# Kernel tuning notes

Measured on AMD Instinct MI355X. Metric: run time of the kernel, lower is better.

The kernel has to match this reference:

```python
import jax, jax.numpy as jnp
import numpy as np

GROUP_SIZES = [16, 16, 16, 16]
K = 2
TEMPERATURE = 1.0
NEG = float(np.finfo(np.float32).min)  # torch.finfo(dtype).min


def setup_inputs() -> dict:
    key = jax.random.key(0)
    k1, k2, k3 = jax.random.split(key, 3)
    B, S, D, E, G = 8, 4096, 1024, 64, len(GROUP_SIZES)
    x = jax.random.normal(k1, (B, S, D), dtype=jnp.float32)
    W_group = jax.random.normal(k2, (G, D), dtype=jnp.float32) * 0.02
    W_expert = jax.random.normal(k3, (E, D), dtype=jnp.float32) * 0.02
    return {"x": x, "W_group": W_group, "W_expert": W_expert}


def reference(x, W_group, W_expert):
    E = W_expert.shape[0]
    # group id of each expert (contiguous ranges) -- static
    expert_group = jnp.asarray(np.repeat(np.arange(len(GROUP_SIZES)), GROUP_SIZES))  # [E]

    # gate logits (no bias), temperature scaling
    expert_logits = jnp.einsum('bsd,ed->bse', x, W_expert) * (1.0 / TEMPERATURE)  # [B,S,E]
    group_logits = jnp.einsum('bsd,gd->bsg', x, W_group)                          # [B,S,G]
    group_probs = jax.nn.softmax(group_logits, axis=-1)
    g_idx = jnp.argmax(group_probs, axis=-1)                                      # [B,S]

    # mask experts outside the selected group's contiguous range
    mask = expert_group[None, None, :] != g_idx[..., None]                        # [B,S,E] bool
    mdt = mask.astype(expert_logits.dtype)
    masked_logits = mdt * NEG + (1.0 - mdt) * expert_logits

    probs_full = jax.nn.softmax(masked_logits, axis=-1)                           # [B,S,E]
    topk_vals, idx = jax.lax.top_k(masked_logits, K)                              # [B,S,K]
    scores = jax.nn.softmax(topk_vals, axis=-1)

    # aux stats (no_grad in original)
    importance = jax.lax.stop_gradient(jnp.mean(probs_full, axis=(0, 1)))         # [E]
    counts = jnp.zeros((E,), probs_full.dtype).at[idx.reshape(-1)].add(1.0)       # [E]
    load = counts / jnp.maximum(jnp.sum(counts), 1.0)
    return (idx, scores, probs_full, importance, load)
```

## Files before the change

kernel.cpp:

```cpp
#include <hip/hip_runtime.h>
#include <math.h>

#define TOKENS   32768
#define DDIM     1024
#define TPB      64
#define NBLOCKS  (TOKENS / TPB)

#define OFF_SCORES 65536
#define OFF_PROBS  131072
#define OFF_IMP    2228224
#define OFF_LOAD   2228288

#define NSLOT 16

typedef __attribute__((ext_vector_type(8))) short  short8;
typedef __attribute__((ext_vector_type(4))) float  f32x4;
typedef __attribute__((ext_vector_type(4))) int    intx4;

__device__ __attribute__((aligned(16))) short wfrag[32 * 5 * 3 * 64 * 8];

__device__ inline unsigned rne_hi(float x) {
  unsigned u = __float_as_uint(x);
  unsigned r = u + 0x7fffu + ((u >> 16) & 1u);
  return r & 0xffff0000u;
}

__device__ inline void split3(const float* xv, short8& f1, short8& f2, short8& f3) {
  int o1[4], o2[4], o3[4];
  #pragma unroll
  for (int p = 0; p < 4; ++p) {
    float x0 = xv[2*p], x1 = xv[2*p+1];
    unsigned h0 = rne_hi(x0), h1 = rne_hi(x1);
    o1[p] = (int)((h0 >> 16) | (h1 & 0xffff0000u));
    float r0 = x0 - __uint_as_float(h0);
    float r1 = x1 - __uint_as_float(h1);
    unsigned g0 = rne_hi(r0), g1 = rne_hi(r1);
    o2[p] = (int)((g0 >> 16) | (g1 & 0xffff0000u));
    float s0 = r0 - __uint_as_float(g0);
    float s1 = r1 - __uint_as_float(g1);
    unsigned w0 = rne_hi(s0), w1 = rne_hi(s1);
    o3[p] = (int)((w0 >> 16) | (w1 & 0xffff0000u));
  }
  intx4 t1 = {o1[0], o1[1], o1[2], o1[3]};
  intx4 t2 = {o2[0], o2[1], o2[2], o2[3]};
  intx4 t3 = {o3[0], o3[1], o3[2], o3[3]};
  f1 = __builtin_bit_cast(short8, t1);
  f2 = __builtin_bit_cast(short8, t2);
  f3 = __builtin_bit_cast(short8, t3);
}

__global__ void prep_kernel(const float* __restrict__ Wg, const float* __restrict__ We,
                            float* __restrict__ ws) {
  const int nt   = blockIdx.x >> 5;
  const int ks   = blockIdx.x & 31;
  const int lane = threadIdx.x & 63;
  if (blockIdx.x < 32) ws[blockIdx.x * 64 + lane] = 0.f;
  const int row  = nt * 16 + (lane & 15);
  const int k0   = ks * 32 + (lane >> 4) * 8;
  float xv[8];
  #pragma unroll
  for (int j = 0; j < 8; ++j) {
    float v = 0.f;
    if (row < 64)      v = We[(size_t)row * DDIM + k0 + j];
    else if (row < 68) v = Wg[(size_t)(row - 64) * DDIM + k0 + j];
    xv[j] = v;
  }
  short8 f1, f2, f3;
  split3(xv, f1, f2, f3);
  short8* dst = (short8*)wfrag + (((size_t)ks * 5 + nt) * 3) * 64 + lane;
  dst[0]   = f1;
  dst[64]  = f2;
  dst[128] = f3;
}

__global__ __launch_bounds__(256)
__attribute__((amdgpu_waves_per_eu(2)))
void router_kernel(const float* __restrict__ x,
                   float* __restrict__ out,
                   float* __restrict__ ws) {
  __shared__ __attribute__((aligned(16))) char smem[61440 + 256];
  float*  el     = (float*)smem;
  short8* bstage = (short8*)smem;
  int*    cnt    = (int*)(smem + 61440);
  const int tid    = threadIdx.x;
  const int lane   = tid & 63;
  const int wv     = tid >> 6;
  const int khalf  = wv >> 1;
  const int mhalf  = wv & 1;
  const int quad   = lane >> 4;
  const int m      = lane & 15;
  const int tokblk = blockIdx.x * TPB;

  if (tid < 64) cnt[tid] = 0;

  const float* apb = x + (size_t)(tokblk + mhalf * 32 + m) * DDIM + khalf * 512 + quad * 8;
  const short8* wsrc = (const short8*)wfrag;

  f32x4 ahi[2][5], alo[2][5];
  #pragma unroll
  for (int mt = 0; mt < 2; ++mt)
    #pragma unroll
    for (int nt = 0; nt < 5; ++nt) { ahi[mt][nt] = 0.f; alo[mt][nt] = 0.f; }

  float4 cur[4], nxt[4];
  #pragma unroll
  for (int mt = 0; mt < 2; ++mt) {
    const float* p = apb + (size_t)(mt * 16) * DDIM;
    cur[mt * 2]     = *(const float4*)(p);
    cur[mt * 2 + 1] = *(const float4*)(p + 4);
  }

  {
    short8 breg[8];
    #pragma unroll
    for (int j = 0; j < 8; ++j) {
      const int c = wv + 4 * j;
      if (c < 30) {
        const int ksg = (c < 15) ? 0 : 16;
        const int fr  = (c < 15) ? c : c - 15;
        breg[j] = wsrc[((size_t)ksg * 15 + fr) * 64 + lane];
      }
    }
    #pragma unroll
    for (int j = 0; j < 8; ++j) {
      const int c = wv + 4 * j;
      if (c < 30) bstage[c * 64 + lane] = breg[j];
    }
  }
  __syncthreads();

  for (int ks = 0; ks < 16; ++ks) {
    const int pb = ks & 1;
    short8 breg[8];
    if (ks < 15) {
      #pragma unroll
      for (int j = 0; j < 8; ++j) {
        const int c = wv + 4 * j;
        if (c < 30) {
          const int ksg = (c < 15) ? (ks + 1) : (16 + ks + 1);
          const int fr  = (c < 15) ? c : c - 15;
          breg[j] = wsrc[((size_t)ksg * 15 + fr) * 64 + lane];
        }
      }
    }
    const int kpf = (ks + 1 < 16) ? (ks + 1) : 15;
    #pragma unroll
    for (int mt = 0; mt < 2; ++mt) {
      const float* p = apb + (size_t)(mt * 16) * DDIM + kpf * 32;
      nxt[mt * 2]     = *(const float4*)(p);
      nxt[mt * 2 + 1] = *(const float4*)(p + 4);
    }
    short8 fa[2][3];
    #pragma unroll
    for (int mt = 0; mt < 2; ++mt) {
      float av[8] = {cur[mt*2].x, cur[mt*2].y, cur[mt*2].z, cur[mt*2].w,
                     cur[mt*2+1].x, cur[mt*2+1].y, cur[mt*2+1].z, cur[mt*2+1].w};
      split3(av, fa[mt][0], fa[mt][1], fa[mt][2]);
    }
    const short8* bbase = &bstage[(size_t)pb * 1920 + (size_t)khalf * 15 * 64 + lane];
    short8 fb0 = bbase[0], fb1 = bbase[64], fb2 = bbase[128];
    #pragma unroll
    for (int nt = 0; nt < 5; ++nt) {
      short8 n0, n1, n2;
      if (nt < 4) {
        n0 = bbase[(nt + 1) * 192];
        n1 = bbase[(nt + 1) * 192 + 64];
        n2 = bbase[(nt + 1) * 192 + 128];
      }
      #pragma unroll
      for (int mt = 0; mt < 2; ++mt) {
        ahi[mt][nt] = __builtin_amdgcn_mfma_f32_16x16x32_bf16(fa[mt][0], fb0, ahi[mt][nt], 0, 0, 0);
        f32x4 c = alo[mt][nt];
        c = __builtin_amdgcn_mfma_f32_16x16x32_bf16(fa[mt][0], fb1, c, 0, 0, 0);
        c = __builtin_amdgcn_mfma_f32_16x16x32_bf16(fa[mt][1], fb0, c, 0, 0, 0);
        c = __builtin_amdgcn_mfma_f32_16x16x32_bf16(fa[mt][1], fb1, c, 0, 0, 0);
        c = __builtin_amdgcn_mfma_f32_16x16x32_bf16(fa[mt][0], fb2, c, 0, 0, 0);
        c = __builtin_amdgcn_mfma_f32_16x16x32_bf16(fa[mt][2], fb0, c, 0, 0, 0);
        c = __builtin_amdgcn_mfma_f32_16x16x32_bf16(fa[mt][1], fb2, c, 0, 0, 0);
        c = __builtin_amdgcn_mfma_f32_16x16x32_bf16(fa[mt][2], fb1, c, 0, 0, 0);
        alo[mt][nt] = c;
      }
      if (nt < 4) { fb0 = n0; fb1 = n1; fb2 = n2; }
    }
    if (ks < 15) {
      #pragma unroll
      for (int j = 0; j < 8; ++j) {
        const int c = wv + 4 * j;
        if (c < 30) bstage[(size_t)(pb ^ 1) * 1920 + c * 64 + lane] = breg[j];
      }
      __syncthreads();
    }
    #pragma unroll
    for (int i = 0; i < 4; ++i) cur[i] = nxt[i];
  }

  if (khalf == 1) {
    #pragma unroll
    for (int mt = 0; mt < 2; ++mt)
      #pragma unroll
      for (int nt = 0; nt < 5; ++nt)
        #pragma unroll
        for (int r = 0; r < 4; ++r)
          el[(mhalf * 32 + mt * 16 + quad * 4 + r) * 88 + nt * 16 + m] = ahi[mt][nt][r] + alo[mt][nt][r];
  }
  __syncthreads();
  if (khalf == 0) {
    #pragma unroll
    for (int mt = 0; mt < 2; ++mt)
      #pragma unroll
      for (int nt = 0; nt < 5; ++nt)
        #pragma unroll
        for (int r = 0; r < 4; ++r) {
          const int idx = (mhalf * 32 + mt * 16 + quad * 4 + r) * 88 + nt * 16 + m;
          el[idx] += ahi[mt][nt][r] + alo[mt][nt][r];
        }
  }
  __syncthreads();

  if (tid < TPB) {
    const int t = tid;
    float* row = el + t * 88;
    const float g0 = row[64], g1 = row[65], g2 = row[66], g3 = row[67];
    int g = 0; float gb = g0;
    if (g1 > gb) { g = 1; gb = g1; }
    if (g2 > gb) { g = 2; gb = g2; }
    if (g3 > gb) { g = 3; gb = g3; }
    const int base = g << 4;
    float l[16];
    #pragma unroll
    for (int e = 0; e < 16; ++e) l[e] = row[base + e];
    int i1 = 0; float v1 = l[0];
    #pragma unroll
    for (int e = 1; e < 16; ++e) if (l[e] > v1) { i1 = e; v1 = l[e]; }
    int i2 = -1; float v2 = 0.f;
    #pragma unroll
    for (int e = 0; e < 16; ++e) {
      if (e == i1) continue;
      if (i2 < 0 || l[e] > v2) { i2 = e; v2 = l[e]; }
    }
    float pr[16]; float s = 0.f;
    #pragma unroll
    for (int e = 0; e < 16; ++e) { pr[e] = expf(l[e] - v1); s += pr[e]; }
    const float inv = 1.f / s;
    #pragma unroll
    for (int c = 0; c < 64; ++c) row[c] = 0.f;
    #pragma unroll
    for (int e = 0; e < 16; ++e) row[base + e] = pr[e] * inv;
    const size_t T = (size_t)tokblk + t;
    out[2*T]     = (float)(base + i1);
    out[2*T + 1] = (float)(base + i2);
    const float e2 = expf(v2 - v1);
    const float si = 1.f / (1.f + e2);
    out[OFF_SCORES + 2*T]     = si;
    out[OFF_SCORES + 2*T + 1] = e2 * si;
    atomicAdd(&cnt[base + i1], 1);
    atomicAdd(&cnt[base + i2], 1);
  }
  __syncthreads();

  for (int i = tid; i < TPB * 64; i += 256) {
    const int t = i >> 6, c = i & 63;
    out[OFF_PROBS + (((size_t)(tokblk + t)) << 6) + c] = el[t * 88 + c];
  }
  if (tid < 64) {
    const int e = tid;
    float s = 0.f;
    #pragma unroll 4
    for (int t = 0; t < TPB; ++t) s += el[t * 88 + e];
    const int slot = (blockIdx.x & (NSLOT - 1)) * 128;
    atomicAdd(&ws[slot + e], s);
    atomicAdd(&ws[slot + 64 + e], (float)cnt[e]);
  }
}

__global__ void finalize_kernel(const float* __restrict__ ws, float* __restrict__ out) {
  const int e = threadIdx.x;
  if (e < 64) {
    float imp = 0.f, cf = 0.f;
    #pragma unroll
    for (int s = 0; s < NSLOT; ++s) {
      imp += ws[s * 128 + e];
      cf  += ws[s * 128 + 64 + e];
    }
    out[OFF_IMP  + e] = imp * (1.0f / 32768.0f);
    out[OFF_LOAD + e] = cf  * (1.0f / 65536.0f);
  }
}

extern "C" void kernel_launch(void* const* d_in, const int* in_sizes, int n_in,
                              void* d_out, int out_size, void* d_ws, size_t ws_size,
                              hipStream_t stream) {
  (void)in_sizes; (void)n_in; (void)out_size; (void)ws_size;
  const float* x  = (const float*)d_in[0];
  const float* Wg = (const float*)d_in[1];
  const float* We = (const float*)d_in[2];
  float* out = (float*)d_out;
  float* ws  = (float*)d_ws;
  hipLaunchKernelGGL(prep_kernel, dim3(160), dim3(64), 0, stream, Wg, We, ws);
  hipLaunchKernelGGL(router_kernel, dim3(NBLOCKS), dim3(256), 0, stream, x, out, ws);
  hipLaunchKernelGGL(finalize_kernel, dim3(1), dim3(64), 0, stream, ws, out);
}
```

Before: 206.5 us.

## Stage weight fragments with direct global-to-LDS loads and fuse finalize via last-block counter

Pads the weight fragment layout to 16 fragments per k-step so each wave can issue 16-byte global_load_lds copies straight into shared memory. This replaces the register round-trip of load-then-store staging. It also folds the finalize kernel into the router kernel: a last-block-done atomic counter lets the final block reduce the importance and load slots, which saves one kernel launch. The costs are a slightly larger LDS footprint, an extra zero fragment to load, and added atomic/fence synchronisation at kernel end.

```diff
diff --git a/kernel.cpp b/kernel.cpp
--- a/kernel.cpp
+++ b/kernel.cpp
@@ -17,7 +17,13 @@
 typedef __attribute__((ext_vector_type(4))) float  f32x4;
 typedef __attribute__((ext_vector_type(4))) int    intx4;
 
-__device__ __attribute__((aligned(16))) short wfrag[32 * 5 * 3 * 64 * 8];
+__device__ __attribute__((aligned(16))) short wfrag[32 * 16 * 64 * 8];
+
+__device__ inline void stage16(const void* g, void* l) {
+  __builtin_amdgcn_global_load_lds(
+      (const __attribute__((address_space(1))) void*)g,
+      (__attribute__((address_space(3))) void*)l, 16, 0, 0);
+}
 
 __device__ inline unsigned rne_hi(float x) {
   unsigned u = __float_as_uint(x);
@@ -55,6 +61,7 @@
   const int ks   = blockIdx.x & 31;
   const int lane = threadIdx.x & 63;
   if (blockIdx.x < 32) ws[blockIdx.x * 64 + lane] = 0.f;
+  if (blockIdx.x == 0 && threadIdx.x == 0) ((unsigned*)ws)[2048] = 0u;
   const int row  = nt * 16 + (lane & 15);
   const int k0   = ks * 32 + (lane >> 4) * 8;
   float xv[8];
@@ -67,10 +74,14 @@
   }
   short8 f1, f2, f3;
   split3(xv, f1, f2, f3);
-  short8* dst = (short8*)wfrag + (((size_t)ks * 5 + nt) * 3) * 64 + lane;
+  short8* dst = (short8*)wfrag + ((size_t)ks * 16 + nt * 3) * 64 + lane;
   dst[0]   = f1;
   dst[64]  = f2;
   dst[128] = f3;
+  if (nt == 4) {
+    short8 z = {};
+    ((short8*)wfrag)[((size_t)ks * 16 + 15) * 64 + lane] = z;
+  }
 }
 
 __global__ __launch_bounds__(256)
@@ -78,10 +89,10 @@
 void router_kernel(const float* __restrict__ x,
                    float* __restrict__ out,
                    float* __restrict__ ws) {
-  __shared__ __attribute__((aligned(16))) char smem[61440 + 256];
+  __shared__ __attribute__((aligned(16))) char smem[65536 + 384];
   float*  el     = (float*)smem;
   short8* bstage = (short8*)smem;
-  int*    cnt    = (int*)(smem + 61440);
+  int*    cnt    = (int*)(smem + 65536);
   const int tid    = threadIdx.x;
   const int lane   = tid & 63;
   const int wv     = tid >> 6;
@@ -94,7 +105,7 @@
   if (tid < 64) cnt[tid] = 0;
 
   const float* apb = x + (size_t)(tokblk + mhalf * 32 + m) * DDIM + khalf * 512 + quad * 8;
-  const short8* wsrc = (const short8*)wfrag;
+  const short* wsrc = wfrag;
 
   f32x4 ahi[2][5], alo[2][5];
   #pragma unroll
@@ -110,45 +121,33 @@
     cur[mt * 2 + 1] = *(const float4*)(p + 4);
   }
 
-  {
-    short8 breg[8];
-    #pragma unroll
-    for (int j = 0; j < 8; ++j) {
-      const int c = wv + 4 * j;
-      if (c < 30) {
-        const int ksg = (c < 15) ? 0 : 16;
-        const int fr  = (c < 15) ? c : c - 15;
-        breg[j] = wsrc[((size_t)ksg * 15 + fr) * 64 + lane];
-      }
-    }
-    #pragma unroll
-    for (int j = 0; j < 8; ++j) {
-      const int c = wv + 4 * j;
-      if (c < 30) bstage[c * 64 + lane] = breg[j];
-    }
+  #pragma unroll
+  for (int j = 0; j < 8; ++j) {
+    const int c = wv + 4 * j;
+    const int G = ((c < 16) ? 0 : 16) * 16 + (c & 15) * 1 + ((c < 16) ? 0 : 0) * 0;
+    const int gstep = (c < 16) ? 0 : 16;
+    const short* gs = wsrc + ((size_t)(gstep * 16 + (c & 15)) * 64 + lane) * 8;
+    stage16(gs, smem + c * 1024);
+    (void)G;
   }
   __syncthreads();
 
   for (int ks = 0; ks < 16; ++ks) {
     const int pb = ks & 1;
-    short8 breg[8];
     if (ks < 15) {
       #pragma unroll
       for (int j = 0; j < 8; ++j) {
         const int c = wv + 4 * j;
-        if (c < 30) {
-          const int ksg = (c < 15) ? (ks + 1) : (16 + ks + 1);
-          const int fr  = (c < 15) ? c : c - 15;
-          breg[j] = wsrc[((size_t)ksg * 15 + fr) * 64 + lane];
-        }
+        const int gstep = ((c < 16) ? 0 : 16) + ks + 1;
+        const short* gs = wsrc + ((size_t)(gstep * 16 + (c & 15)) * 64 + lane) * 8;
+        stage16(gs, smem + (pb ^ 1) * 32768 + c * 1024);
       }
-    }
-    const int kpf = (ks + 1 < 16) ? (ks + 1) : 15;
-    #pragma unroll
-    for (int mt = 0; mt < 2; ++mt) {
-      const float* p = apb + (size_t)(mt * 16) * DDIM + kpf * 32;
-      nxt[mt * 2]     = *(const float4*)(p);
-      nxt[mt * 2 + 1] = *(const float4*)(p + 4);
+      #pragma unroll
+      for (int mt = 0; mt < 2; ++mt) {
+        const float* p = apb + (size_t)(mt * 16) * DDIM + (ks + 1) * 32;
+        nxt[mt * 2]     = *(const float4*)(p);
+        nxt[mt * 2 + 1] = *(const float4*)(p + 4);
+      }
     }
     short8 fa[2][3];
     #pragma unroll
@@ -157,7 +156,7 @@
                      cur[mt*2+1].x, cur[mt*2+1].y, cur[mt*2+1].z, cur[mt*2+1].w};
       split3(av, fa[mt][0], fa[mt][1], fa[mt][2]);
     }
-    const short8* bbase = &bstage[(size_t)pb * 1920 + (size_t)khalf * 15 * 64 + lane];
+    const short8* bbase = &bstage[(size_t)pb * 2048 + (size_t)khalf * 16 * 64 + lane];
     short8 fb0 = bbase[0], fb1 = bbase[64], fb2 = bbase[128];
     #pragma unroll
     for (int nt = 0; nt < 5; ++nt) {
@@ -183,15 +182,10 @@
       if (nt < 4) { fb0 = n0; fb1 = n1; fb2 = n2; }
     }
     if (ks < 15) {
-      #pragma unroll
-      for (int j = 0; j < 8; ++j) {
-        const int c = wv + 4 * j;
-        if (c < 30) bstage[(size_t)(pb ^ 1) * 1920 + c * 64 + lane] = breg[j];
-      }
       __syncthreads();
-    }
-    #pragma unroll
-    for (int i = 0; i < 4; ++i) cur[i] = nxt[i];
+      #pragma unroll
+      for (int i = 0; i < 4; ++i) cur[i] = nxt[i];
+    }
   }
 
   if (khalf == 1) {
@@ -271,16 +265,22 @@
     atomicAdd(&ws[slot + e], s);
     atomicAdd(&ws[slot + 64 + e], (float)cnt[e]);
   }
-}
-
-__global__ void finalize_kernel(const float* __restrict__ ws, float* __restrict__ out) {
-  const int e = threadIdx.x;
-  if (e < 64) {
+
+  __syncthreads();
+  if (tid == 0) {
+    __threadfence();
+    unsigned prev = __hip_atomic_fetch_add((unsigned*)(ws + 2048), 1u,
+                                           __ATOMIC_ACQ_REL, __HIP_MEMORY_SCOPE_AGENT);
+    cnt[64] = (prev == (unsigned)(NBLOCKS - 1)) ? 1 : 0;
+  }
+  __syncthreads();
+  if (cnt[64] && tid < 64) {
+    const int e = tid;
     float imp = 0.f, cf = 0.f;
     #pragma unroll
     for (int s = 0; s < NSLOT; ++s) {
-      imp += ws[s * 128 + e];
-      cf  += ws[s * 128 + 64 + e];
+      imp += __hip_atomic_load(&ws[s * 128 + e],      __ATOMIC_RELAXED, __HIP_MEMORY_SCOPE_AGENT);
+      cf  += __hip_atomic_load(&ws[s * 128 + 64 + e], __ATOMIC_RELAXED, __HIP_MEMORY_SCOPE_AGENT);
     }
     out[OFF_IMP  + e] = imp * (1.0f / 32768.0f);
     out[OFF_LOAD + e] = cf  * (1.0f / 65536.0f);
@@ -298,5 +298,4 @@
   float* ws  = (float*)d_ws;
   hipLaunchKernelGGL(prep_kernel, dim3(160), dim3(64), 0, stream, Wg, We, ws);
   hipLaunchKernelGGL(router_kernel, dim3(NBLOCKS), dim3(256), 0, stream, x, out, ws);
-  hipLaunchKernelGGL(finalize_kernel, dim3(1), dim3(64), 0, stream, ws, out);
-}
+}
```

After: 228.9 us. 10.8% more time.
